# Kernel optimization log

Measured on AMD Instinct MI355X. Metric: run time of the kernel, lower is better.

Reference implementation:

```python
import jax, jax.numpy as jnp
import numpy as np
import math

D_MODEL = 1024
N_HEADS = 16
D_KV = 64
NUM_BUCKETS = 32
MAX_DISTANCE = 128
BATCH = 4
SEQ = 2048


def _relative_position_bucket(relative_position, num_buckets=NUM_BUCKETS, max_distance=MAX_DISTANCE):
    # bidirectional=True (encoder)
    num_buckets //= 2
    relative_buckets = (relative_position > 0).astype(jnp.int32) * num_buckets
    rp = jnp.abs(relative_position)
    max_exact = num_buckets // 2
    is_small = rp < max_exact
    rp_safe = jnp.maximum(rp, 1)  # avoid log(0); masked by is_small anyway
    rp_if_large = max_exact + (
        jnp.log(rp_safe.astype(jnp.float32) / max_exact)
        / math.log(max_distance / max_exact)
        * (num_buckets - max_exact)
    ).astype(jnp.int32)
    rp_if_large = jnp.minimum(rp_if_large, num_buckets - 1)
    relative_buckets += jnp.where(is_small, rp, rp_if_large)
    return relative_buckets


def compute_bias(rel_bias, q_len, k_len):
    context = jnp.arange(q_len)[:, None]
    memory = jnp.arange(k_len)[None, :]
    buckets = _relative_position_bucket(memory - context)  # [q, k]
    values = rel_bias[buckets]                              # [q, k, h]
    return jnp.transpose(values, (2, 0, 1))[None]           # [1, h, q, k]


def setup_inputs() -> dict:
    key = jax.random.key(0)
    ks = jax.random.split(key, 6)
    s = 1.0 / math.sqrt(D_MODEL)
    return {
        "hidden_states": jax.random.normal(ks[0], (BATCH, SEQ, D_MODEL), jnp.float32),
        "wq": jax.random.normal(ks[1], (D_MODEL, N_HEADS * D_KV), jnp.float32) * s,
        "wk": jax.random.normal(ks[2], (D_MODEL, N_HEADS * D_KV), jnp.float32) * s,
        "wv": jax.random.normal(ks[3], (D_MODEL, N_HEADS * D_KV), jnp.float32) * s,
        "wo": jax.random.normal(ks[4], (N_HEADS * D_KV, D_MODEL), jnp.float32) * s,
        "rel_bias": jax.random.normal(ks[5], (NUM_BUCKETS, N_HEADS), jnp.float32) * 0.5,
    }


def reference(hidden_states, wq, wk, wv, wo, rel_bias):
    B, S, _ = hidden_states.shape

    def shape(x):  # [B,S,H*Dk] -> [B,H,S,Dk]
        return x.reshape(B, S, N_HEADS, D_KV).transpose(0, 2, 1, 3)

    q = shape(hidden_states @ wq)
    k = shape(hidden_states @ wk)
    v = shape(hidden_states @ wv)

    # NOTE: T5 does NOT scale by 1/sqrt(d_kv)
    scores = jnp.einsum("bhqd,bhkd->bhqk", q, k)
    position_bias = compute_bias(rel_bias, S, S)  # [1,H,S,S]
    scores = scores + position_bias
    attn = jax.nn.softmax(scores.astype(jnp.float32), axis=-1).astype(scores.dtype)
    ctx = jnp.einsum("bhqk,bhkd->bhqd", attn, v)
    ctx = ctx.transpose(0, 2, 1, 3).reshape(B, S, N_HEADS * D_KV)
    return ctx @ wo
```

## Files before the change

kernel.cpp:

```cpp
#include <hip/hip_runtime.h>
#include <hip/hip_bf16.h>

typedef unsigned short u16;
typedef unsigned int   u32;
typedef __bf16 bf16x8 __attribute__((ext_vector_type(8)));
typedef float  f32x4  __attribute__((ext_vector_type(4)));
typedef u16    u16x8  __attribute__((ext_vector_type(8)));
typedef u16    u16x4  __attribute__((ext_vector_type(4)));

#define MFMA16(a,b,c) __builtin_amdgcn_mfma_f32_16x16x32_bf16(a,b,c,0,0,0)
#define LOG2E 1.4426950408889634f

__device__ __forceinline__ u16 f2b(float f) {
    u32 u = __builtin_bit_cast(u32, f);
    u32 r = (u + 0x7FFFu + ((u >> 16) & 1u)) >> 16;
    return (u16)r;
}

typedef const __attribute__((address_space(1))) u32* gaddr_t;
typedef __attribute__((address_space(3))) u32*       laddr_t;
__device__ __forceinline__ void gl_lds16(const void* g, void* l) {
    __builtin_amdgcn_global_load_lds((gaddr_t)g, (laddr_t)l, 16, 0, 0);
}

__global__ __launch_bounds__(256) void prep_kernel(
        const float* __restrict__ H, const float* __restrict__ wq,
        const float* __restrict__ wk, const float* __restrict__ wv,
        const float* __restrict__ wo, const float* __restrict__ rel_bias,
        u16* __restrict__ Hb, u16* __restrict__ Wt, u16* __restrict__ Wot,
        float* __restrict__ tab) {
    __shared__ u16 tile[64 * 72];
    int bi = blockIdx.x;
    int t = threadIdx.x;
    if (bi < 4096) {
        int i = (bi * 256 + t) * 8;
        float4 a = *(const float4*)(H + i);
        float4 b = *(const float4*)(H + i + 4);
        u16x8 o = { f2b(a.x), f2b(a.y), f2b(a.z), f2b(a.w),
                    f2b(b.x), f2b(b.y), f2b(b.z), f2b(b.w) };
        *(u16x8*)(Hb + i) = o;
    } else if (bi < 5120) {
        int g2 = bi - 4096;
        int g = g2 >> 8, rem = g2 & 255;
        int n0 = (rem >> 4) * 64, k0 = (rem & 15) * 64;
        const float* src = (g == 0) ? wq : (g == 1) ? wk : (g == 2) ? wv : wo;
        u16* dst = (g < 3) ? (Wt + g * 1048576) : Wot;
#pragma unroll
        for (int rr = 0; rr < 4; ++rr) {
            int idx = rr * 256 + t;
            int kr = idx >> 4, c = idx & 15;
            float4 v = *(const float4*)(src + (k0 + kr) * 1024 + n0 + c * 4);
            u16x4 o = { f2b(v.x), f2b(v.y), f2b(v.z), f2b(v.w) };
            *(u16x4*)&tile[kr * 72 + c * 4] = o;
        }
        __syncthreads();
#pragma unroll
        for (int rr = 0; rr < 2; ++rr) {
            int idx = rr * 256 + t;
            int n = idx >> 3, c = idx & 7;
            u16x8 o;
#pragma unroll
            for (int j = 0; j < 8; ++j) o[j] = tile[(c * 8 + j) * 72 + n];
            *(u16x8*)(dst + (n0 + n) * 1024 + k0 + c * 8) = o;
        }
    } else {
        int i = (bi - 5120) * 256 + t;
        int h = i >> 12;
        int idx = i & 4095;
        int delta = idx - 2048;
        int bucket = (delta > 0) ? 16 : 0;
        int rp = delta < 0 ? -delta : delta;
        if (rp < 8) {
            bucket += rp;
        } else {
            double v = log((double)rp / 8.0) / log(16.0) * 8.0;
            int tt = (int)v;
            int b2 = 8 + tt;
            bucket += (b2 < 15) ? b2 : 15;
        }
        tab[h * 4096 + idx] = rel_bias[bucket * 16 + h] * LOG2E;
    }
}

template <int MODE>
__global__ __launch_bounds__(256) void gemm_bt(
        const u16* __restrict__ A, const u16* __restrict__ Bt, int K, int N,
        u16* __restrict__ q_out, u16* __restrict__ k_out, u16* __restrict__ v_out,
        float* __restrict__ f_out) {
    __shared__ u16 As[128 * 32];
    __shared__ u16 Bs[128 * 32];
    __shared__ u16 vt_tile[MODE == 0 ? 128 * 136 : 1];
    int t = threadIdx.x;
    int lane = t & 63, w = t >> 6;
    int wm = w & 1, wn = w >> 1;
    int ln = lane & 15, quad = lane >> 4;
    int m0 = blockIdx.x * 128, n0 = blockIdx.y * 128;
    const u16* Ab = A + m0 * K;
    const u16* Bb = Bt + n0 * K;
    f32x4 acc[4][4] = {};
    int nk = K >> 5;
    for (int kt = 0; kt < nk; ++kt) {
        int k0 = kt * 32;
#pragma unroll
        for (int rr = 0; rr < 2; ++rr) {
            int idx = rr * 256 + t;
            int row = idx >> 2, c = (idx & 3) ^ (row & 3);
            gl_lds16(Ab + row * K + k0 + c * 8, ((char*)As) + idx * 16);
            gl_lds16(Bb + row * K + k0 + c * 8, ((char*)Bs) + idx * 16);
        }
        __syncthreads();
        bf16x8 af[4], bfr[4];
#pragma unroll
        for (int mb = 0; mb < 4; ++mb) {
            int row = wm * 64 + mb * 16 + ln;
            af[mb] = *(const bf16x8*)&As[row * 32 + ((quad ^ (row & 3)) << 3)];
        }
#pragma unroll
        for (int nb = 0; nb < 4; ++nb) {
            int row = wn * 64 + nb * 16 + ln;
            bfr[nb] = *(const bf16x8*)&Bs[row * 32 + ((quad ^ (row & 3)) << 3)];
        }
#pragma unroll
        for (int mb = 0; mb < 4; ++mb)
#pragma unroll
            for (int nb = 0; nb < 4; ++nb)
                acc[mb][nb] = MFMA16(af[mb], bfr[nb], acc[mb][nb]);
        __syncthreads();
    }
    if (MODE == 0 && n0 >= 2048) {
#pragma unroll
        for (int mb = 0; mb < 4; ++mb)
#pragma unroll
            for (int nb = 0; nb < 4; ++nb)
#pragma unroll
                for (int r = 0; r < 4; ++r) {
                    int np = wn * 64 + nb * 16 + ln;
                    int mp = wm * 64 + mb * 16 + quad * 4 + r;
                    vt_tile[np * 136 + mp] = f2b(acc[mb][nb][r]);
                }
        __syncthreads();
        int h0 = (n0 >> 6) & 15;
        int b = m0 >> 11;
        int s0 = m0 & 2047;
#pragma unroll
        for (int j = 0; j < 8; ++j) {
            int e = j * 256 + t;
            int d_all = e >> 4;
            int sc = e & 15;
            int hh = h0 + (d_all >> 6);
            int d = d_all & 63;
            u16x8 val = *(const u16x8*)&vt_tile[d_all * 136 + sc * 8];
            *(u16x8*)(v_out + (b * 16 + hh) * 131072 + d * 2048 + s0 + sc * 8) = val;
        }
    } else {
#pragma unroll
        for (int mb = 0; mb < 4; ++mb)
#pragma unroll
            for (int nb = 0; nb < 4; ++nb)
#pragma unroll
                for (int r = 0; r < 4; ++r) {
                    int m = m0 + wm * 64 + mb * 16 + quad * 4 + r;
                    int n = n0 + wn * 64 + nb * 16 + ln;
                    float v = acc[mb][nb][r];
                    if (MODE == 0) {
                        int which = n >> 10, h = (n >> 6) & 15, d = n & 63;
                        int b = m >> 11, s = m & 2047;
                        u16* dst = (which == 0) ? q_out : k_out;
                        float scale = (which == 0) ? LOG2E : 1.0f;
                        dst[(((b << 4) + h) * 2048 + s) * 64 + d] = f2b(v * scale);
                    } else {
                        f_out[m * N + n] = v;
                    }
                }
    }
}

__global__ __launch_bounds__(256, 3) void attn_kernel(
        const u16* __restrict__ Qb, const u16* __restrict__ Kb,
        const u16* __restrict__ Vt, const float* __restrict__ bias_tab,
        u16* __restrict__ ctx) {
    __shared__ u16 Ks[128 * 64];
    __shared__ u16 Vs[64 * 128];
    __shared__ u16 Ps[4][16 * 64];
    __shared__ float sb[2176];
    int t = threadIdx.x;
    int lane = t & 63, w = t >> 6;
    int ln = lane & 15, quad = lane >> 4;
    int bh = blockIdx.x >> 5;
    int qtile = blockIdx.x & 31;
    int h = bh & 15, b = bh >> 4;
    int q0 = qtile * 64;

    float chi = bias_tab[h * 4096 + 2048 + 1500];
    float clo = bias_tab[h * 4096 + 2048 - 1500];

    const float* tb = bias_tab + h * 4096 + (1985 - q0);
    for (int i = t; i < 2175; i += 256) sb[i] = tb[i];

    int qa = q0 + w * 16 + ln;
    const u16* qptr = Qb + (bh * 2048 + qa) * 64 + quad * 8;
    bf16x8 qf0 = *(const bf16x8*)(qptr);
    bf16x8 qf1 = *(const bf16x8*)(qptr + 32);

    const u16* Kbase = Kb + bh * 2048 * 64;
    const u16* Vbase = Vt + bh * 64 * 2048;

    f32x4 oacc[4] = {};
    float l_i = 0.0f;
    int cb_base = 63 - w * 16 + quad * 4 - ln;
    int swl = ln & 7;

    for (int kt = 0; kt < 16; ++kt) {
        int kb0 = kt * 128;
#pragma unroll
        for (int it = 0; it < 4; ++it) {
            int idx = it * 256 + t;
            int row = idx >> 3, c = (idx & 7) ^ (row & 7);
            gl_lds16(Kbase + (kb0 + row) * 64 + c * 8, ((char*)Ks) + idx * 16);
        }
#pragma unroll
        for (int it = 0; it < 4; ++it) {
            int idx = it * 256 + t;
            int row = idx >> 4, c = (idx & 15) ^ (row & 7);
            gl_lds16(Vbase + row * 2048 + kb0 + c * 8, ((char*)Vs) + idx * 16);
        }
        __syncthreads();

        f32x4 sacc[8];
        int diff = kb0 - q0;
        if (diff >= 192 || diff <= -256) {
            float c0 = (diff > 0) ? chi : clo;
            f32x4 ci = {c0, c0, c0, c0};
#pragma unroll
            for (int nb = 0; nb < 8; ++nb) {
                int key = nb * 16 + ln;
                int sw = key & 7;
                bf16x8 kf0 = *(const bf16x8*)&Ks[key * 64 + ((quad ^ sw) << 3)];
                bf16x8 kf1 = *(const bf16x8*)&Ks[key * 64 + (((quad ^ 4) ^ sw) << 3)];
                f32x4 scc = MFMA16(kf0, qf0, ci);
                sacc[nb] = MFMA16(kf1, qf1, scc);
            }
        } else {
            int cb = kb0 + cb_base;
#pragma unroll
            for (int nb = 0; nb < 8; ++nb) {
                int key = nb * 16 + ln;
                int sw = key & 7;
                const float* bp = &sb[cb + nb * 16];
                f32x4 ci = {bp[0], bp[1], bp[2], bp[3]};
                bf16x8 kf0 = *(const bf16x8*)&Ks[key * 64 + ((quad ^ sw) << 3)];
                bf16x8 kf1 = *(const bf16x8*)&Ks[key * 64 + (((quad ^ 4) ^ sw) << 3)];
                f32x4 scc = MFMA16(kf0, qf0, ci);
                sacc[nb] = MFMA16(kf1, qf1, scc);
            }
        }

        float p[8][4];
        float ls0 = 0.f, ls1 = 0.f, ls2 = 0.f, ls3 = 0.f;
#pragma unroll
        for (int nb = 0; nb < 8; ++nb) {
            float e0 = __builtin_amdgcn_exp2f(sacc[nb][0]);
            float e1 = __builtin_amdgcn_exp2f(sacc[nb][1]);
            float e2 = __builtin_amdgcn_exp2f(sacc[nb][2]);
            float e3 = __builtin_amdgcn_exp2f(sacc[nb][3]);
            p[nb][0] = e0; p[nb][1] = e1; p[nb][2] = e2; p[nb][3] = e3;
            ls0 += e0; ls1 += e1; ls2 += e2; ls3 += e3;
        }
        l_i += (ls0 + ls1) + (ls2 + ls3);

        u16* pw = &Ps[w][0];
#pragma unroll
        for (int half = 0; half < 2; ++half) {
#pragma unroll
            for (int nbh = 0; nbh < 4; ++nbh) {
                int nb = half * 4 + nbh;
                u32 a0 = __builtin_bit_cast(u32, p[nb][0]) + 0x8000u;
                u32 a1 = __builtin_bit_cast(u32, p[nb][1]) + 0x8000u;
                u32 a2 = __builtin_bit_cast(u32, p[nb][2]) + 0x8000u;
                u32 a3 = __builtin_bit_cast(u32, p[nb][3]) + 0x8000u;
                u32 lo = __builtin_amdgcn_perm(a1, a0, 0x07060302);
                u32 hi = __builtin_amdgcn_perm(a3, a2, 0x07060302);
                int c = nbh * 2 + (quad >> 1);
                u32* dst = (u32*)&pw[ln * 64 + ((c ^ swl) << 3) + (quad & 1) * 4];
                dst[0] = lo;
                dst[1] = hi;
            }
#pragma unroll
            for (int kc = 0; kc < 2; ++kc) {
                bf16x8 pf = *(const bf16x8*)&pw[ln * 64 + (((kc * 4 + quad) ^ swl) << 3)];
#pragma unroll
                for (int nb = 0; nb < 4; ++nb) {
                    int d = nb * 16 + ln;
                    int vc = (half * 8 + kc * 4 + quad) ^ (d & 7);
                    bf16x8 vf = *(const bf16x8*)&Vs[d * 128 + (vc << 3)];
                    oacc[nb] = MFMA16(pf, vf, oacc[nb]);
                }
            }
        }
        __syncthreads();
    }

    l_i += __shfl_xor(l_i, 16);
    l_i += __shfl_xor(l_i, 32);
    float linv = 1.0f / l_i;
#pragma unroll
    for (int r = 0; r < 4; ++r) {
        float lr = __shfl(linv, quad * 4 + r);
        int q = q0 + w * 16 + quad * 4 + r;
#pragma unroll
        for (int nb = 0; nb < 4; ++nb)
            ctx[(b * 2048 + q) * 1024 + h * 64 + nb * 16 + ln] = f2b(oacc[nb][r] * lr);
    }
}

extern "C" void kernel_launch(void* const* d_in, const int* in_sizes, int n_in,
                              void* d_out, int out_size, void* d_ws, size_t ws_size,
                              hipStream_t stream) {
    const float* H   = (const float*)d_in[0];
    const float* wq  = (const float*)d_in[1];
    const float* wk  = (const float*)d_in[2];
    const float* wv  = (const float*)d_in[3];
    const float* wo  = (const float*)d_in[4];
    const float* rel = (const float*)d_in[5];
    float* out = (float*)d_out;

    char* ws = (char*)d_ws;
    u16* Hb    = (u16*)(ws);
    u16* Wt    = (u16*)(ws + 16777216);
    u16* Wot   = (u16*)(ws + 23068672);
    u16* Qb    = (u16*)(ws + 25165824);
    u16* Kb    = (u16*)(ws + 41943040);
    u16* Vt    = (u16*)(ws + 58720256);
    float* bias_tab = (float*)(ws + 75497472);
    u16* ctx = Hb;

    prep_kernel<<<5376, 256, 0, stream>>>(H, wq, wk, wv, wo, rel, Hb, Wt, Wot, bias_tab);
    gemm_bt<0><<<dim3(64, 24), 256, 0, stream>>>(Hb, Wt, 1024, 3072, Qb, Kb, Vt, nullptr);
    attn_kernel<<<2048, 256, 0, stream>>>(Qb, Kb, Vt, bias_tab, ctx);
    gemm_bt<1><<<dim3(64, 8), 256, 0, stream>>>(ctx, Wot, 1024, 1024, nullptr, nullptr, nullptr, out);
}
```

Before: 302.7 us.

## Double-buffer K/V tiles in attention with 64-key tiles and prefetch

Splits the attention key loop into 64-key tiles held in two shared-memory buffers, issuing async global-to-LDS loads for the next tile while computing on the current one. This hides load latency behind the MFMA work instead of stalling at a barrier each iteration. It also shrinks the bias table staged in shared memory to a window relative to the diagonal, uses hardware packed bf16 conversion for P, and raises wave priority around MFMA blocks. The single barrier per iteration has to cover both the prefetch and the buffer reuse, and smaller tiles mean more loop iterations.

```diff
diff --git a/kernel.cpp b/kernel.cpp
--- a/kernel.cpp
+++ b/kernel.cpp
@@ -179,10 +179,10 @@
         const u16* __restrict__ Qb, const u16* __restrict__ Kb,
         const u16* __restrict__ Vt, const float* __restrict__ bias_tab,
         u16* __restrict__ ctx) {
-    __shared__ u16 Ks[128 * 64];
-    __shared__ u16 Vs[64 * 128];
+    __shared__ u16 Ks[2][64 * 64];
+    __shared__ u16 Vs[2][64 * 64];
     __shared__ u16 Ps[4][16 * 64];
-    __shared__ float sb[2176];
+    __shared__ float sb[384];
     int t = threadIdx.x;
     int lane = t & 63, w = t >> 6;
     int ln = lane & 15, quad = lane >> 4;
@@ -194,8 +194,8 @@
     float chi = bias_tab[h * 4096 + 2048 + 1500];
     float clo = bias_tab[h * 4096 + 2048 - 1500];
 
-    const float* tb = bias_tab + h * 4096 + (1985 - q0);
-    for (int i = t; i < 2175; i += 256) sb[i] = tb[i];
+    const float* tb = bias_tab + h * 4096 + 1857;
+    for (int i = t; i < 384; i += 256) sb[i] = tb[i];
 
     int qa = q0 + w * 16 + ln;
     const u16* qptr = Qb + (bh * 2048 + qa) * 64 + quad * 8;
@@ -207,58 +207,75 @@
 
     f32x4 oacc[4] = {};
     float l_i = 0.0f;
-    int cb_base = 63 - w * 16 + quad * 4 - ln;
+    int cb2_base = 191 - w * 16 + quad * 4 - ln;
     int swl = ln & 7;
 
-    for (int kt = 0; kt < 16; ++kt) {
-        int kb0 = kt * 128;
-#pragma unroll
-        for (int it = 0; it < 4; ++it) {
-            int idx = it * 256 + t;
-            int row = idx >> 3, c = (idx & 7) ^ (row & 7);
-            gl_lds16(Kbase + (kb0 + row) * 64 + c * 8, ((char*)Ks) + idx * 16);
-        }
-#pragma unroll
-        for (int it = 0; it < 4; ++it) {
-            int idx = it * 256 + t;
-            int row = idx >> 4, c = (idx & 15) ^ (row & 7);
-            gl_lds16(Vbase + row * 2048 + kb0 + c * 8, ((char*)Vs) + idx * 16);
-        }
-        __syncthreads();
-
-        f32x4 sacc[8];
+#pragma unroll
+    for (int it = 0; it < 2; ++it) {
+        int idx = it * 256 + t;
+        int row = idx >> 3, c = (idx & 7) ^ (row & 7);
+        gl_lds16(Kbase + row * 64 + c * 8, ((char*)&Ks[0][0]) + idx * 16);
+        gl_lds16(Vbase + row * 2048 + c * 8, ((char*)&Vs[0][0]) + idx * 16);
+    }
+    __syncthreads();
+
+#pragma unroll 2
+    for (int kt = 0; kt < 32; ++kt) {
+        int cur = kt & 1;
+        int kb0 = kt * 64;
+
+        if (kt < 31) {
+            int nxt = kb0 + 64;
+#pragma unroll
+            for (int it = 0; it < 2; ++it) {
+                int idx = it * 256 + t;
+                int row = idx >> 3, c = (idx & 7) ^ (row & 7);
+                gl_lds16(Kbase + (nxt + row) * 64 + c * 8,
+                         ((char*)&Ks[cur ^ 1][0]) + idx * 16);
+                gl_lds16(Vbase + row * 2048 + nxt + c * 8,
+                         ((char*)&Vs[cur ^ 1][0]) + idx * 16);
+            }
+        }
+        const u16* Kc = &Ks[cur][0];
+        const u16* Vc = &Vs[cur][0];
+
+        f32x4 sacc[4];
         int diff = kb0 - q0;
-        if (diff >= 192 || diff <= -256) {
+        if (diff >= 192 || diff <= -192) {
             float c0 = (diff > 0) ? chi : clo;
             f32x4 ci = {c0, c0, c0, c0};
-#pragma unroll
-            for (int nb = 0; nb < 8; ++nb) {
+            __builtin_amdgcn_s_setprio(1);
+#pragma unroll
+            for (int nb = 0; nb < 4; ++nb) {
                 int key = nb * 16 + ln;
                 int sw = key & 7;
-                bf16x8 kf0 = *(const bf16x8*)&Ks[key * 64 + ((quad ^ sw) << 3)];
-                bf16x8 kf1 = *(const bf16x8*)&Ks[key * 64 + (((quad ^ 4) ^ sw) << 3)];
+                bf16x8 kf0 = *(const bf16x8*)&Kc[key * 64 + ((quad ^ sw) << 3)];
+                bf16x8 kf1 = *(const bf16x8*)&Kc[key * 64 + (((quad ^ 4) ^ sw) << 3)];
                 f32x4 scc = MFMA16(kf0, qf0, ci);
                 sacc[nb] = MFMA16(kf1, qf1, scc);
             }
+            __builtin_amdgcn_s_setprio(0);
         } else {
-            int cb = kb0 + cb_base;
-#pragma unroll
-            for (int nb = 0; nb < 8; ++nb) {
+            int cb = diff + cb2_base;
+            __builtin_amdgcn_s_setprio(1);
+#pragma unroll
+            for (int nb = 0; nb < 4; ++nb) {
                 int key = nb * 16 + ln;
                 int sw = key & 7;
                 const float* bp = &sb[cb + nb * 16];
                 f32x4 ci = {bp[0], bp[1], bp[2], bp[3]};
-                bf16x8 kf0 = *(const bf16x8*)&Ks[key * 64 + ((quad ^ sw) << 3)];
-                bf16x8 kf1 = *(const bf16x8*)&Ks[key * 64 + (((quad ^ 4) ^ sw) << 3)];
+                bf16x8 kf0 = *(const bf16x8*)&Kc[key * 64 + ((quad ^ sw) << 3)];
+                bf16x8 kf1 = *(const bf16x8*)&Kc[key * 64 + (((quad ^ 4) ^ sw) << 3)];
                 f32x4 scc = MFMA16(kf0, qf0, ci);
                 sacc[nb] = MFMA16(kf1, qf1, scc);
             }
-        }
-
-        float p[8][4];
+            __builtin_amdgcn_s_setprio(0);
+        }
+
+        float p[4][4];
         float ls0 = 0.f, ls1 = 0.f, ls2 = 0.f, ls3 = 0.f;
 #pragma unroll
-        for (int nb = 0; nb < 8; ++nb) {
+        for (int nb = 0; nb < 4; ++nb) {
             float e0 = __builtin_amdgcn_exp2f(sacc[nb][0]);
             float e1 = __builtin_amdgcn_exp2f(sacc[nb][1]);
             float e2 = __builtin_amdgcn_exp2f(sacc[nb][2]);
@@ -270,32 +287,28 @@
 
         u16* pw = &Ps[w][0];
 #pragma unroll
-        for (int half = 0; half < 2; ++half) {
-#pragma unroll
-            for (int nbh = 0; nbh < 4; ++nbh) {
-                int nb = half * 4 + nbh;
-                u32 a0 = __builtin_bit_cast(u32, p[nb][0]) + 0x8000u;
-                u32 a1 = __builtin_bit_cast(u32, p[nb][1]) + 0x8000u;
-                u32 a2 = __builtin_bit_cast(u32, p[nb][2]) + 0x8000u;
-                u32 a3 = __builtin_bit_cast(u32, p[nb][3]) + 0x8000u;
-                u32 lo = __builtin_amdgcn_perm(a1, a0, 0x07060302);
-                u32 hi = __builtin_amdgcn_perm(a3, a2, 0x07060302);
-                int c = nbh * 2 + (quad >> 1);
-                u32* dst = (u32*)&pw[ln * 64 + ((c ^ swl) << 3) + (quad & 1) * 4];
-                dst[0] = lo;
-                dst[1] = hi;
+        for (int nb = 0; nb < 4; ++nb) {
+            u32 lo, hi;
+            asm("v_cvt_pk_bf16_f32 %0, %1, %2" : "=v"(lo) : "v"(p[nb][0]), "v"(p[nb][1]));
+            asm("v_cvt_pk_bf16_f32 %0, %1, %2" : "=v"(hi) : "v"(p[nb][2]), "v"(p[nb][3]));
+            int c = nb * 2 + (quad >> 1);
+            u32* dst = (u32*)&pw[ln * 64 + ((c ^ swl) << 3) + (quad & 1) * 4];
+            dst[0] = lo;
+            dst[1] = hi;
+        }
+
+#pragma unroll
+        for (int kc = 0; kc < 2; ++kc) {
+            bf16x8 pf = *(const bf16x8*)&pw[ln * 64 + (((kc * 4 + quad) ^ swl) << 3)];
+            __builtin_amdgcn_s_setprio(1);
+#pragma unroll
+            for (int nb = 0; nb < 4; ++nb) {
+                int d = nb * 16 + ln;
+                int vc = (kc * 4 + quad) ^ (d & 7);
+                bf16x8 vf = *(const bf16x8*)&Vc[d * 64 + (vc << 3)];
+                oacc[nb] = MFMA16(pf, vf, oacc[nb]);
             }
-#pragma unroll
-            for (int kc = 0; kc < 2; ++kc) {
-                bf16x8 pf = *(const bf16x8*)&pw[ln * 64 + (((kc * 4 + quad) ^ swl) << 3)];
-#pragma unroll
-                for (int nb = 0; nb < 4; ++nb) {
-                    int d = nb * 16 + ln;
-                    int vc = (half * 8 + kc * 4 + quad) ^ (d & 7);
-                    bf16x8 vf = *(const bf16x8*)&Vs[d * 128 + (vc << 3)];
-                    oacc[nb] = MFMA16(pf, vf, oacc[nb]);
-                }
-            }
+            __builtin_amdgcn_s_setprio(0);
         }
         __syncthreads();
     }
```

After: 307.7 us. About the same (+1.7%).
